# Performance work log

Measured on AMD Instinct MI355X. Metric: run time of the kernel, lower is better.

The kernel has to match this reference:

```python
import jax, jax.numpy as jnp
import numpy as np

# CSSA config (index=0): H=W=64, strip windows h_spa=64, w_spa=8, heads=4, C=64
B, HW, C, HEADS = 32, 64, 64, 4
HS, WS = 64, 8          # h_spa, w_spa
HD = C // HEADS          # head_dim = 16
WIN = HS * WS            # 512 tokens per window
SCALE = HD ** -0.5


def setup_inputs() -> dict:
    key = jax.random.key(0)
    k1, k2, k3 = jax.random.split(key, 3)
    qkv = jax.random.normal(k1, (3, B, HW * HW, C), dtype=jnp.float32)
    w_conv = jax.random.normal(k2, (C, 1, 3, 3), dtype=jnp.float32) * 0.1
    b_conv = jax.random.normal(k3, (C,), dtype=jnp.float32) * 0.1
    return {"qkv": qkv, "w_conv": w_conv, "b_conv": b_conv}


def _to_img(x):
    # [B, N, C] -> [B, C, H, W]
    return jnp.transpose(x.reshape(B, HW, HW, C), (0, 3, 1, 2))


def _img2window_heads(x):
    img = _to_img(x)
    img = img.reshape(B, C, HW // HS, HS, HW // WS, WS)
    win = jnp.transpose(img, (0, 2, 4, 3, 5, 1)).reshape(-1, WIN, C)
    return jnp.transpose(win.reshape(-1, WIN, HEADS, HD), (0, 2, 1, 3))


def _v_windows(x):
    # [B, N, C] -> [B*nWin, C, h_spa, w_spa] (image-layout windows for conv)
    img = _to_img(x)
    img = img.reshape(B, C, HW // HS, HS, HW // WS, WS)
    return jnp.transpose(img, (0, 2, 4, 1, 3, 5)).reshape(-1, C, HS, WS)


def reference(qkv, w_conv, b_conv):
    q, k, v = qkv[0], qkv[1], qkv[2]
    qh = _img2window_heads(q) * SCALE
    kh = _img2window_heads(k)
    vw = _v_windows(v)                           # [Bw, C, HS, WS]
    # depthwise 3x3 conv LePE
    lepe = jax.lax.conv_general_dilated(
        vw, w_conv, window_strides=(1, 1), padding=((1, 1), (1, 1)),
        feature_group_count=C,
        dimension_numbers=("NCHW", "OIHW", "NCHW")) + b_conv[None, :, None, None]
    Bw = vw.shape[0]
    lepe = jnp.transpose(lepe.reshape(Bw, HEADS, HD, WIN), (0, 1, 3, 2))
    vh = jnp.transpose(vw.reshape(Bw, HEADS, HD, WIN), (0, 1, 3, 2))
    attn = jax.nn.softmax(jnp.einsum("whqd,whkd->whqk", qh, kh), axis=-1)
    x = jnp.einsum("whqk,whkd->whqd", attn, vh) + lepe
    x = jnp.transpose(x, (0, 2, 1, 3)).reshape(Bw, WIN, C)
    # window2spa
    x = x.reshape(B, HW // HS, HW // WS, HS, WS, C)
    x = jnp.transpose(x, (0, 1, 3, 2, 4, 5)).reshape(B, HW * HW, C)
    return x
```

## Files before the change

kernel.cpp:

```cpp
#include <hip/hip_runtime.h>
#include <stdint.h>

#define KSTR2 20
#define VSTR  520

typedef __attribute__((ext_vector_type(4))) short          short4v;
typedef __attribute__((ext_vector_type(4))) float          f32x4;
typedef __attribute__((ext_vector_type(4))) unsigned short us4;
typedef __bf16 bf2_t __attribute__((ext_vector_type(2)));

__device__ __forceinline__ float bf2f(unsigned short u) {
    union { unsigned int i; float f; } x; x.i = ((unsigned int)u) << 16; return x.f;
}
__device__ __forceinline__ unsigned int pk2bf(float lo, float hi) {
#if __has_builtin(__builtin_amdgcn_cvt_pk_bf16_f32)
    union { bf2_t v; unsigned int u; } c;
    c.v = __builtin_amdgcn_cvt_pk_bf16_f32(lo, hi);
    return c.u;
#else
    union { float f; unsigned int u; } a, b; a.f = lo; b.f = hi;
    return __builtin_amdgcn_perm(b.u + 0x8000u, a.u + 0x8000u, 0x07060302u);
#endif
}
__device__ __forceinline__ short4v pk4bf(float a, float b, float c, float d) {
    union { short4v s; unsigned int u[2]; } p;
    p.u[0] = pk2bf(a, b);
    p.u[1] = pk2bf(c, d);
    return p.s;
}

__global__ __launch_bounds__(512, 6)
void CSSA_69355131896243_kernel(const float* __restrict__ qkv,
                                const float* __restrict__ wconv,
                                const float* __restrict__ bconv,
                                float* __restrict__ out)
{
    __shared__ unsigned short Kl[512 * KSTR2];
    __shared__ unsigned short Vt[16 * VSTR];
    __shared__ float Wl[144];
    __shared__ float Bl[16];

    const int tid  = threadIdx.x;
    const int wave = tid >> 6, lane = tid & 63, quad = lane >> 4, l15 = lane & 15;

    const int bid  = blockIdx.x;
    const int x    = bid & 7, s = (bid >> 3) & 7, y = bid >> 6;
    const int head = s & 3, qh = s >> 2;
    const int win  = x * 32 + y;
    const int b    = win >> 3, wx = win & 7;
    const int hc   = head * 16;

    const size_t ONE  = (size_t)32 * 4096 * 64;
    const size_t base = ((size_t)b * 4096 + (size_t)wx * 8) * 64;
    const float* gQ = qkv + base;
    const float* gK = qkv + ONE + base;
    const float* gV = qkv + 2 * ONE + base;

    {
        const int c4 = tid & 3;
        const int t0 = tid >> 2;
        #pragma unroll
        for (int r = 0; r < 4; ++r) {
            const int t = r * 128 + t0;
            const size_t goff = (size_t)(t >> 3) * 4096 + (size_t)(t & 7) * 64 + hc + c4 * 4;
            f32x4 kd = *(const f32x4*)(gK + goff);
            union { us4 v; unsigned int u[2]; } kb;
            kb.u[0] = pk2bf(kd[0], kd[1]);
            kb.u[1] = pk2bf(kd[2], kd[3]);
            *(us4*)(&Kl[t * KSTR2 + c4 * 4]) = kb.v;
        }
        const int d = tid & 15;
        #pragma unroll
        for (int r = 0; r < 4; ++r) {
            const int g = (tid >> 4) + r * 32;
            const float* src = gV + (size_t)(g >> 1) * 4096 + (size_t)((g & 1) * 4) * 64 + hc + d;
            const float v0 = src[0], v1 = src[64], v2 = src[128], v3 = src[192];
            union { us4 v; unsigned int u[2]; } vb;
            vb.u[0] = pk2bf(v0, v1);
            vb.u[1] = pk2bf(v2, v3);
            *(us4*)(&Vt[d * VSTR + g * 4]) = vb.v;
        }
    }
    if (tid < 144) Wl[tid] = wconv[head * 144 + tid];
    if (tid < 16)  Bl[tid] = bconv[hc + tid];

    const float SCL = 0.25f * 1.44269504088896341f;
    const int q0 = qh * 256 + wave * 32;
    short4v qf[2];
    #pragma unroll
    for (int t = 0; t < 2; ++t) {
        const int q = q0 + t * 16 + l15;
        f32x4 qv = *(const f32x4*)(gQ + (size_t)(q >> 3) * 4096 + (size_t)(q & 7) * 64 + hc + quad * 4);
        qf[t] = pk4bf(qv[0] * SCL, qv[1] * SCL, qv[2] * SCL, qv[3] * SCL);
    }
    __syncthreads();

    f32x4 acc[2];
    float lp[2];
    #pragma unroll
    for (int t = 0; t < 2; ++t) { acc[t] = (f32x4)0.0f; lp[t] = 0.0f; }

    #pragma unroll 4
    for (int c = 0; c < 32; ++c) {
        const short4v kf = *(const short4v*)(&Kl[(c * 16 + l15) * KSTR2 + quad * 4]);
        const short4v vf = *(const short4v*)(&Vt[l15 * VSTR + c * 16 + quad * 4]);
        #pragma unroll
        for (int t = 0; t < 2; ++t) {
            f32x4 sc = __builtin_amdgcn_mfma_f32_16x16x16bf16_1k(kf, qf[t], (f32x4)0.0f, 0, 0, 0);
            const float p0 = __builtin_amdgcn_exp2f(sc[0]);
            const float p1 = __builtin_amdgcn_exp2f(sc[1]);
            const float p2 = __builtin_amdgcn_exp2f(sc[2]);
            const float p3 = __builtin_amdgcn_exp2f(sc[3]);
            lp[t] += (p0 + p1) + (p2 + p3);
            acc[t] = __builtin_amdgcn_mfma_f32_16x16x16bf16_1k(vf, pk4bf(p0, p1, p2, p3), acc[t], 0, 0, 0);
        }
    }

    float linv[2];
    #pragma unroll
    for (int t = 0; t < 2; ++t) {
        float v = lp[t];
        v += __shfl_xor(v, 16, 64);
        v += __shfl_xor(v, 32, 64);
        linv[t] = __builtin_amdgcn_rcpf(v);
    }

    #pragma unroll
    for (int j = 0; j < 4; ++j) {
        const int d = quad * 4 + j;
        float w9[9];
        #pragma unroll
        for (int o = 0; o < 9; ++o) w9[o] = Wl[d * 9 + o];
        const float bs = Bl[d];
        const unsigned short* vrow = &Vt[d * VSTR];
        #pragma unroll
        for (int t = 0; t < 2; ++t) {
            const int q = q0 + t * 16 + l15;
            const int yy0 = q >> 3, xx0 = l15 & 7;
            float lep = bs;
            #pragma unroll
            for (int dy = 0; dy < 3; ++dy) {
                #pragma unroll
                for (int dx = 0; dx < 3; ++dx) {
                    const int yy = yy0 + dy - 1, xx = xx0 + dx - 1;
                    const bool ok = ((unsigned)yy < 64u) && ((unsigned)xx < 8u);
                    const int tt = (q + (dy - 1) * 8 + (dx - 1)) & 511;
                    lep += (ok ? w9[dy * 3 + dx] : 0.0f) * bf2f(vrow[tt]);
                }
            }
            acc[t][j] = acc[t][j] * linv[t] + lep;
        }
    }
    float* gO = out + base;
    #pragma unroll
    for (int t = 0; t < 2; ++t) {
        const int q = q0 + t * 16 + l15;
        *(f32x4*)(gO + (size_t)(q >> 3) * 4096 + (size_t)(q & 7) * 64 + hc + quad * 4) = acc[t];
    }
}

extern "C" void kernel_launch(void* const* d_in, const int* in_sizes, int n_in,
                              void* d_out, int out_size, void* d_ws, size_t ws_size,
                              hipStream_t stream) {
    const float* qkv   = (const float*)d_in[0];
    const float* wconv = (const float*)d_in[1];
    const float* bconv = (const float*)d_in[2];
    float* outp = (float*)d_out;
    hipLaunchKernelGGL(CSSA_69355131896243_kernel, dim3(2048), dim3(512), 0, stream,
                       qkv, wconv, bconv, outp);
}
```

Measured before the change: 184.0 us.

## Prefetch K/V fragments, compute softmax row sums via MFMA, pad V for branchless LePE

Software-pipelines the attention loop by loading the next chunk's K and V fragments before computing the current one, and raises wave priority around the MFMA/exp block. The per-lane scalar sum of exp values plus the cross-lane shuffles are replaced by an extra MFMA against a ones vector, which yields the row sums directly. V rows in LDS get zero padding on both sides, so the depthwise conv reads need no vertical bounds checks or wraparound masking, and horizontal masking is folded into the weights once. This trades more MFMA work and a slightly larger LDS footprint for fewer VALU ops and shorter dependency chains.

```diff
diff --git a/kernel.cpp b/kernel.cpp
--- a/kernel.cpp
+++ b/kernel.cpp
@@ -2,7 +2,7 @@
 #include <stdint.h>
 
 #define KSTR2 20
-#define VSTR  520
+#define VSTR  552
 
 typedef __attribute__((ext_vector_type(4))) short          short4v;
 typedef __attribute__((ext_vector_type(4))) float          f32x4;
@@ -78,7 +78,12 @@
             union { us4 v; unsigned int u[2]; } vb;
             vb.u[0] = pk2bf(v0, v1);
             vb.u[1] = pk2bf(v2, v3);
-            *(us4*)(&Vt[d * VSTR + g * 4]) = vb.v;
+            *(us4*)(&Vt[d * VSTR + 16 + g * 4]) = vb.v;
+        }
+        if (tid < 160) {
+            const int row = tid / 10, seg = tid % 10;
+            const int off = (seg < 4) ? seg * 4 : 528 + (seg - 4) * 4;
+            *(us4*)(&Vt[row * VSTR + off]) = (us4){0, 0, 0, 0};
         }
     }
     if (tid < 144) Wl[tid] = wconv[head * 144 + tid];
@@ -95,15 +100,21 @@
     }
     __syncthreads();
 
-    f32x4 acc[2];
-    float lp[2];
+    f32x4 acc[2], lsum[2];
     #pragma unroll
-    for (int t = 0; t < 2; ++t) { acc[t] = (f32x4)0.0f; lp[t] = 0.0f; }
+    for (int t = 0; t < 2; ++t) { acc[t] = (f32x4)0.0f; lsum[t] = (f32x4)0.0f; }
+    const short4v ones = {(short)0x3F80, (short)0x3F80, (short)0x3F80, (short)0x3F80};
 
+    const unsigned short* Kbase = &Kl[l15 * KSTR2 + quad * 4];
+    const unsigned short* Vbase = &Vt[l15 * VSTR + 16 + quad * 4];
+    short4v kf = *(const short4v*)(Kbase);
+    short4v vf = *(const short4v*)(Vbase);
     #pragma unroll 4
     for (int c = 0; c < 32; ++c) {
-        const short4v kf = *(const short4v*)(&Kl[(c * 16 + l15) * KSTR2 + quad * 4]);
-        const short4v vf = *(const short4v*)(&Vt[l15 * VSTR + c * 16 + quad * 4]);
+        const int cn = (c + 1) & 31;
+        const short4v kfn = *(const short4v*)(Kbase + cn * 320);
+        const short4v vfn = *(const short4v*)(Vbase + cn * 16);
+        __builtin_amdgcn_s_setprio(1);
         #pragma unroll
         for (int t = 0; t < 2; ++t) {
             f32x4 sc = __builtin_amdgcn_mfma_f32_16x16x16bf16_1k(kf, qf[t], (f32x4)0.0f, 0, 0, 0);
@@ -111,41 +122,39 @@
             const float p1 = __builtin_amdgcn_exp2f(sc[1]);
             const float p2 = __builtin_amdgcn_exp2f(sc[2]);
             const float p3 = __builtin_amdgcn_exp2f(sc[3]);
-            lp[t] += (p0 + p1) + (p2 + p3);
-            acc[t] = __builtin_amdgcn_mfma_f32_16x16x16bf16_1k(vf, pk4bf(p0, p1, p2, p3), acc[t], 0, 0, 0);
+            const short4v pb = pk4bf(p0, p1, p2, p3);
+            lsum[t] = __builtin_amdgcn_mfma_f32_16x16x16bf16_1k(ones, pb, lsum[t], 0, 0, 0);
+            acc[t]  = __builtin_amdgcn_mfma_f32_16x16x16bf16_1k(vf,   pb, acc[t],  0, 0, 0);
         }
+        __builtin_amdgcn_s_setprio(0);
+        kf = kfn; vf = vfn;
     }
 
     float linv[2];
     #pragma unroll
-    for (int t = 0; t < 2; ++t) {
-        float v = lp[t];
-        v += __shfl_xor(v, 16, 64);
-        v += __shfl_xor(v, 32, 64);
-        linv[t] = __builtin_amdgcn_rcpf(v);
-    }
+    for (int t = 0; t < 2; ++t) linv[t] = __builtin_amdgcn_rcpf(lsum[t][0]);
 
+    const int xx0 = l15 & 7;
+    const bool mx0 = (xx0 >= 1), mx2 = (xx0 <= 6);
     #pragma unroll
     for (int j = 0; j < 4; ++j) {
         const int d = quad * 4 + j;
         float w9[9];
         #pragma unroll
         for (int o = 0; o < 9; ++o) w9[o] = Wl[d * 9 + o];
+        w9[0] = mx0 ? w9[0] : 0.0f;  w9[3] = mx0 ? w9[3] : 0.0f;  w9[6] = mx0 ? w9[6] : 0.0f;
+        w9[2] = mx2 ? w9[2] : 0.0f;  w9[5] = mx2 ? w9[5] : 0.0f;  w9[8] = mx2 ? w9[8] : 0.0f;
         const float bs = Bl[d];
-        const unsigned short* vrow = &Vt[d * VSTR];
+        const unsigned short* vrow = &Vt[d * VSTR + 16];
         #pragma unroll
         for (int t = 0; t < 2; ++t) {
             const int q = q0 + t * 16 + l15;
-            const int yy0 = q >> 3, xx0 = l15 & 7;
             float lep = bs;
             #pragma unroll
             for (int dy = 0; dy < 3; ++dy) {
                 #pragma unroll
                 for (int dx = 0; dx < 3; ++dx) {
-                    const int yy = yy0 + dy - 1, xx = xx0 + dx - 1;
-                    const bool ok = ((unsigned)yy < 64u) && ((unsigned)xx < 8u);
-                    const int tt = (q + (dy - 1) * 8 + (dx - 1)) & 511;
-                    lep += (ok ? w9[dy * 3 + dx] : 0.0f) * bf2f(vrow[tt]);
+                    lep += w9[dy * 3 + dx] * bf2f(vrow[q + (dy - 1) * 8 + (dx - 1)]);
                 }
             }
             acc[t][j] = acc[t][j] * linv[t] + lep;
```

Result: slower. 196.0 us (+6.5%).
